# Performance work log

Hardware: AMD Instinct MI355X
Metric: run time of the kernel (lower is better)

## Reference

```python
import jax, jax.numpy as jnp
import numpy as np

SIZE = (64, 64, 64)
NSTEPS = 7
_EPS = 1e-4


def _skew(w):
    z = jnp.zeros_like(w[:, 0])
    return jnp.stack([
        jnp.stack([z, -w[:, 2], w[:, 1]], -1),
        jnp.stack([w[:, 2], z, -w[:, 0]], -1),
        jnp.stack([-w[:, 1], w[:, 0], z], -1)], -2)


def _abc(theta):
    t2 = theta * theta
    small = theta < _EPS
    ts = jnp.where(small, 1.0, theta)
    A = jnp.where(small, 1.0 - t2 / 6.0, jnp.sin(ts) / ts)
    B = jnp.where(small, 0.5 - t2 / 24.0, (1.0 - jnp.cos(ts)) / (ts * ts))
    C = jnp.where(small, 1.0 / 6.0 - t2 / 120.0, (ts - jnp.sin(ts)) / (ts ** 3))
    return A, B, C


def se3_exp(xi):
    # xi: (N,6) = [v | w]; Rodrigues closed form -> (N,4,4)
    v, w = xi[:, :3], xi[:, 3:]
    theta = jnp.linalg.norm(w, axis=-1)
    A, B, C = _abc(theta)
    Wm = _skew(w)
    W2 = Wm @ Wm
    I = jnp.eye(3, dtype=xi.dtype)
    R = I + A[:, None, None] * Wm + B[:, None, None] * W2
    V = I + B[:, None, None] * Wm + C[:, None, None] * W2
    t = jnp.einsum('nij,nj->ni', V, v)
    top = jnp.concatenate([R, t[:, :, None]], -1)
    bottom = jnp.broadcast_to(jnp.array([0., 0., 0., 1.], xi.dtype), (xi.shape[0], 1, 4))
    return jnp.concatenate([top, bottom], 1)


def se3_log(M):
    # M: (N,4,4) -> (N,6) = [v | w]
    R = M[:, :3, :3]
    t = M[:, :3, 3]
    tr = jnp.trace(R, axis1=1, axis2=2)
    cos = jnp.clip((tr - 1.0) * 0.5, -1.0 + 1e-6, 1.0 - 1e-6)
    theta = jnp.arccos(cos)
    small = theta < _EPS
    ts = jnp.where(small, 1.0, theta)
    t2 = theta * theta
    fac = jnp.where(small, 1.0 + t2 / 6.0, ts / jnp.sin(ts))
    S = 0.5 * (R - jnp.swapaxes(R, 1, 2))
    w = jnp.stack([S[:, 2, 1], S[:, 0, 2], S[:, 1, 0]], -1) * fac[:, None]
    Wm = _skew(w)
    W2 = Wm @ Wm
    A, B, _ = _abc(theta)
    coef = jnp.where(small, 1.0 / 12.0, (1.0 - A / (2.0 * B)) / jnp.where(small, 1.0, t2))
    I = jnp.eye(3, dtype=M.dtype)
    Vinv = I - 0.5 * Wm + coef[:, None, None] * W2
    v = jnp.einsum('nij,nj->ni', Vinv, t)
    return jnp.concatenate([v, w], -1)


def _grid_points():
    # replicates NSETransformer grid: (2*i - (s-1)) / (max(size)-1), flattened (N,3)
    m = float(max(SIZE) - 1)
    ax = [(2.0 * jnp.arange(s, dtype=jnp.float32) - (s - 1)) / m for s in SIZE]
    g = jnp.stack(jnp.meshgrid(*ax, indexing='ij'), -1)  # (D,H,W,3)
    return g.reshape(-1, 3)


def _trilinear(src, coords):
    # src: (C,D,H,W); coords: (N,3) as (x,y,z) in [-1,1]; align_corners=True, border padding
    C, D, H, W = src.shape
    gx = jnp.clip((coords[:, 0] + 1.0) * 0.5 * (W - 1), 0.0, W - 1.0)
    gy = jnp.clip((coords[:, 1] + 1.0) * 0.5 * (H - 1), 0.0, H - 1.0)
    gz = jnp.clip((coords[:, 2] + 1.0) * 0.5 * (D - 1), 0.0, D - 1.0)
    x0 = jnp.floor(gx); y0 = jnp.floor(gy); z0 = jnp.floor(gz)
    fx, fy, fz = gx - x0, gy - y0, gz - z0
    x0i = x0.astype(jnp.int32); x1i = jnp.minimum(x0i + 1, W - 1)
    y0i = y0.astype(jnp.int32); y1i = jnp.minimum(y0i + 1, H - 1)
    z0i = z0.astype(jnp.int32); z1i = jnp.minimum(z0i + 1, D - 1)

    def g(zi, yi, xi):
        return src[:, zi, yi, xi]  # (C,N)

    out = (g(z0i, y0i, x0i) * (1 - fz) * (1 - fy) * (1 - fx)
           + g(z0i, y0i, x1i) * (1 - fz) * (1 - fy) * fx
           + g(z0i, y1i, x0i) * (1 - fz) * fy * (1 - fx)
           + g(z0i, y1i, x1i) * (1 - fz) * fy * fx
           + g(z1i, y0i, x0i) * fz * (1 - fy) * (1 - fx)
           + g(z1i, y0i, x1i) * fz * (1 - fy) * fx
           + g(z1i, y1i, x0i) * fz * fy * (1 - fx)
           + g(z1i, y1i, x1i) * fz * fy * fx)
    return out.T  # (N,C)


def setup_inputs() -> dict:
    key = jax.random.key(0)
    vec = jax.random.normal(key, (1, 6) + SIZE, dtype=jnp.float32) * 0.4
    return {"vec": vec}


def reference(vec):
    D, H, W = SIZE
    scale = 1.0 / (2 ** NSTEPS)
    vec_f = jnp.transpose(vec, (0, 2, 3, 4, 1)).reshape(-1, 6) * scale  # (N,6)
    mulMat = se3_exp(vec_f)  # (N,4,4)
    pts = _grid_points()  # (N,3) in (d0,d1,d2) order
    m = float(max(SIZE) - 1)
    denom = jnp.array([(s - 1) / m for s in SIZE], jnp.float32)
    for _ in range(NSTEPS):
        # SE3.act(mulMat, grid points)
        new_loc = jnp.einsum('nij,nj->ni', mulMat[:, :3, :3], pts) + mulMat[:, :3, 3]
        samp = (new_loc / denom)[:, ::-1]  # reorder [2,1,0] -> (x,y,z)
        src = vec_f.reshape(D, H, W, 6).transpose(3, 0, 1, 2)  # (6,D,H,W)
        interp = _trilinear(src, samp)  # (N,6)
        Mat2 = se3_exp(interp)
        mulMat = Mat2 @ mulMat
        vec_f = se3_log(mulMat)
    return vec_f
```

## Files before the change

### kernel.cpp

```cpp
#include <hip/hip_runtime.h>
#include <math.h>

#define DSZ   64
#define NVOX  (DSZ*DSZ*DSZ)
#define NSTEP 7

__device__ __forceinline__ float rcp_f(float x)  { return __builtin_amdgcn_rcpf(x); }
__device__ __forceinline__ float rsq_f(float x)  { return __builtin_amdgcn_rsqf(x); }

__device__ __forceinline__ void se3_exp_dev(const float xi[6], float R[9], float t[3]) {
    float vx = xi[0], vy = xi[1], vz = xi[2];
    float wx = xi[3], wy = xi[4], wz = xi[5];
    float t2 = wx*wx + wy*wy + wz*wz;
    float t2c = fmaxf(t2, 1e-20f);
    float it    = rsq_f(t2c);
    float theta = t2c*it;
    float s = __sinf(theta), c = __cosf(theta);
    float it2 = it*it;
    float A = s*it;
    float B = (1.0f - c)*it2;
    float C = (theta - s)*it2*it;
    bool sm = t2 < 1e-6f;
    A = sm ? 1.0f - t2*(1.0f/6.0f)            : A;
    B = sm ? 0.5f - t2*(1.0f/24.0f)           : B;
    C = sm ? (1.0f/6.0f) - t2*(1.0f/120.0f)   : C;

    float xx = wx*wx, yy = wy*wy, zz = wz*wz;
    float xy = wx*wy, xz = wx*wz, yz = wy*wz;
    R[0] = 1.0f - B*(yy+zz);
    R[1] = -A*wz + B*xy;
    R[2] =  A*wy + B*xz;
    R[3] =  A*wz + B*xy;
    R[4] = 1.0f - B*(xx+zz);
    R[5] = -A*wx + B*yz;
    R[6] = -A*wy + B*xz;
    R[7] =  A*wx + B*yz;
    R[8] = 1.0f - B*(xx+yy);
    float V0 = 1.0f - C*(yy+zz);
    float V1 = -B*wz + C*xy;
    float V2 =  B*wy + C*xz;
    float V3 =  B*wz + C*xy;
    float V4 = 1.0f - C*(xx+zz);
    float V5 = -B*wx + C*yz;
    float V6 = -B*wy + C*xz;
    float V7 =  B*wx + C*yz;
    float V8 = 1.0f - C*(xx+yy);
    t[0] = V0*vx + V1*vy + V2*vz;
    t[1] = V3*vx + V4*vy + V5*vz;
    t[2] = V6*vx + V7*vy + V8*vz;
}

__device__ __forceinline__ void se3_log_dev(const float R[9], const float t[3], float out[6]) {
    float tr = R[0] + R[4] + R[8];
    float cs = (tr - 1.0f)*0.5f;
    cs = fminf(fmaxf(cs, -1.0f + 1e-6f), 1.0f - 1e-6f);
    float theta = acosf(cs);
    float t2 = theta*theta;
    float ss2 = 1.0f - cs*cs;
    float isn = rsq_f(ss2);
    float fac = theta*isn;
    float sn  = ss2*isn;
    float coef = (1.0f - 0.5f*sn*theta*rcp_f(1.0f - cs)) * rcp_f(t2);
    bool sm = theta < 1e-3f;
    fac  = sm ? 1.0f + t2*(1.0f/6.0f) : fac;
    coef = sm ? (1.0f/12.0f)          : coef;

    float wx = 0.5f*(R[7]-R[5])*fac;
    float wy = 0.5f*(R[2]-R[6])*fac;
    float wz = 0.5f*(R[3]-R[1])*fac;
    float xx = wx*wx, yy = wy*wy, zz = wz*wz;
    float xy = wx*wy, xz = wx*wz, yz = wy*wz;
    float V0 = 1.0f - coef*(yy+zz);
    float V1 =  0.5f*wz + coef*xy;
    float V2 = -0.5f*wy + coef*xz;
    float V3 = -0.5f*wz + coef*xy;
    float V4 = 1.0f - coef*(xx+zz);
    float V5 =  0.5f*wx + coef*yz;
    float V6 =  0.5f*wy + coef*xz;
    float V7 = -0.5f*wx + coef*yz;
    float V8 = 1.0f - coef*(xx+yy);
    out[0] = V0*t[0] + V1*t[1] + V2*t[2];
    out[1] = V3*t[0] + V4*t[1] + V5*t[2];
    out[2] = V6*t[0] + V7*t[1] + V8*t[2];
    out[3] = wx; out[4] = wy; out[5] = wz;
}

__global__ __launch_bounds__(256) void init_kernel(const float* __restrict__ in,
                                                   float* __restrict__ vec) {
    int n = blockIdx.x*256 + threadIdx.x;
    const float scale = 1.0f/128.0f;
    float xi[6];
#pragma unroll
    for (int c = 0; c < 6; ++c) xi[c] = in[c*NVOX + n]*scale;
    float2* vp = reinterpret_cast<float2*>(vec + (size_t)n*6);
    vp[0] = make_float2(xi[0], xi[1]);
    vp[1] = make_float2(xi[2], xi[3]);
    vp[2] = make_float2(xi[4], xi[5]);
}

__global__ __launch_bounds__(256) void step_kernel(const float* __restrict__ vin,
                                                   float* __restrict__ vout) {
    int n = blockIdx.x*256 + threadIdx.x;

    const float2* v2 = reinterpret_cast<const float2*>(vin);
    float2 o0 = v2[n*3], o1 = v2[n*3+1], o2 = v2[n*3+2];
    float xi_own[6] = {o0.x, o0.y, o1.x, o1.y, o2.x, o2.y};
    float Rm[9], tm[3];
    se3_exp_dev(xi_own, Rm, tm);

    int k = n & 63, j = (n >> 6) & 63, i = n >> 12;
    const float inv63 = 1.0f/63.0f;
    float p0 = (float)(2*i - 63)*inv63;
    float p1 = (float)(2*j - 63)*inv63;
    float p2 = (float)(2*k - 63)*inv63;

    float nl0 = Rm[0]*p0 + Rm[1]*p1 + Rm[2]*p2 + tm[0];
    float nl1 = Rm[3]*p0 + Rm[4]*p1 + Rm[5]*p2 + tm[1];
    float nl2 = Rm[6]*p0 + Rm[7]*p1 + Rm[8]*p2 + tm[2];

    float gx = fminf(fmaxf((nl2 + 1.0f)*0.5f*63.0f, 0.0f), 63.0f);
    float gy = fminf(fmaxf((nl1 + 1.0f)*0.5f*63.0f, 0.0f), 63.0f);
    float gz = fminf(fmaxf((nl0 + 1.0f)*0.5f*63.0f, 0.0f), 63.0f);
    float x0f = floorf(gx), y0f = floorf(gy), z0f = floorf(gz);
    float fx = gx - x0f, fy = gy - y0f, fz = gz - z0f;
    int x0 = (int)x0f, y0 = (int)y0f, z0 = (int)z0f;
    int x1 = min(x0 + 1, 63), y1 = min(y0 + 1, 63), z1 = min(z0 + 1, 63);

    float w000 = (1.0f-fz)*(1.0f-fy)*(1.0f-fx);
    float w001 = (1.0f-fz)*(1.0f-fy)*fx;
    float w010 = (1.0f-fz)*fy*(1.0f-fx);
    float w011 = (1.0f-fz)*fy*fx;
    float w100 = fz*(1.0f-fy)*(1.0f-fx);
    float w101 = fz*(1.0f-fy)*fx;
    float w110 = fz*fy*(1.0f-fx);
    float w111 = fz*fy*fx;

    float acc0 = 0.f, acc1 = 0.f, acc2 = 0.f, acc3 = 0.f, acc4 = 0.f, acc5 = 0.f;
#define CORNER(zz_, yy_, xx_, ww_)                                              \
    {                                                                           \
        int b = ((((zz_) << 6) | (yy_)) << 6 | (xx_))*3;                        \
        float2 a = v2[b], bb = v2[b+1], cc = v2[b+2];                           \
        acc0 += (ww_)*a.x;  acc1 += (ww_)*a.y;                                  \
        acc2 += (ww_)*bb.x; acc3 += (ww_)*bb.y;                                 \
        acc4 += (ww_)*cc.x; acc5 += (ww_)*cc.y;                                 \
    }
    CORNER(z0, y0, x0, w000)
    CORNER(z0, y0, x1, w001)
    CORNER(z0, y1, x0, w010)
    CORNER(z0, y1, x1, w011)
    CORNER(z1, y0, x0, w100)
    CORNER(z1, y0, x1, w101)
    CORNER(z1, y1, x0, w110)
    CORNER(z1, y1, x1, w111)
#undef CORNER

    float interp[6] = {acc0, acc1, acc2, acc3, acc4, acc5};
    float R2[9], t2v[3];
    se3_exp_dev(interp, R2, t2v);

    float Rn[9], tn[3];
    Rn[0] = R2[0]*Rm[0] + R2[1]*Rm[3] + R2[2]*Rm[6];
    Rn[1] = R2[0]*Rm[1] + R2[1]*Rm[4] + R2[2]*Rm[7];
    Rn[2] = R2[0]*Rm[2] + R2[1]*Rm[5] + R2[2]*Rm[8];
    Rn[3] = R2[3]*Rm[0] + R2[4]*Rm[3] + R2[5]*Rm[6];
    Rn[4] = R2[3]*Rm[1] + R2[4]*Rm[4] + R2[5]*Rm[7];
    Rn[5] = R2[3]*Rm[2] + R2[4]*Rm[5] + R2[5]*Rm[8];
    Rn[6] = R2[6]*Rm[0] + R2[7]*Rm[3] + R2[8]*Rm[6];
    Rn[7] = R2[6]*Rm[1] + R2[7]*Rm[4] + R2[8]*Rm[7];
    Rn[8] = R2[6]*Rm[2] + R2[7]*Rm[5] + R2[8]*Rm[8];
    tn[0] = R2[0]*tm[0] + R2[1]*tm[1] + R2[2]*tm[2] + t2v[0];
    tn[1] = R2[3]*tm[0] + R2[4]*tm[1] + R2[5]*tm[2] + t2v[1];
    tn[2] = R2[6]*tm[0] + R2[7]*tm[1] + R2[8]*tm[2] + t2v[2];

    float out6[6];
    se3_log_dev(Rn, tn, out6);
    float2* op = reinterpret_cast<float2*>(vout + (size_t)n*6);
    op[0] = make_float2(out6[0], out6[1]);
    op[1] = make_float2(out6[2], out6[3]);
    op[2] = make_float2(out6[4], out6[5]);
}

extern "C" void kernel_launch(void* const* d_in, const int* in_sizes, int n_in,
                              void* d_out, int out_size, void* d_ws, size_t ws_size,
                              hipStream_t stream) {
    (void)in_sizes; (void)n_in; (void)out_size; (void)ws_size;
    const float* in = (const float*)d_in[0];
    float* out  = (float*)d_out;
    float* vecA = (float*)d_ws;

    dim3 blk(256), grid(NVOX/256);
    init_kernel<<<grid, blk, 0, stream>>>(in, vecA);

    const float* cur = vecA;
    for (int s = 1; s <= NSTEP; ++s) {
        float* dst = (s & 1) ? out : vecA;
        step_kernel<<<grid, blk, 0, stream>>>(cur, dst);
        cur = dst;
    }
}
```

Baseline: 72.78 us.

## Fuse init into first step and pad intermediate state to 8 floats

Removes the separate init kernel: the first step now reads the planar input directly and applies the scale after interpolating, so one launch and one full-volume pass are saved. Intermediate buffers are padded to 8 floats per voxel so each corner gather uses two 16-byte float4 loads instead of three float2 loads. The padding raises workspace use and write bandwidth, and the first step's planar gathers touch six separate cache lines per corner.

Measured after the change: 82.07 us. +12.8%, slower.

```diff
diff --git a/kernel.cpp b/kernel.cpp
--- a/kernel.cpp
+++ b/kernel.cpp
@@ -4,6 +4,7 @@
 #define DSZ   64
 #define NVOX  (DSZ*DSZ*DSZ)
 #define NSTEP 7
+#define SCALE (1.0f/128.0f)
 
 __device__ __forceinline__ float rcp_f(float x)  { return __builtin_amdgcn_rcpf(x); }
 __device__ __forceinline__ float rsq_f(float x)  { return __builtin_amdgcn_rsqf(x); }
@@ -85,26 +86,22 @@
     out[3] = wx; out[4] = wy; out[5] = wz;
 }
 
-__global__ __launch_bounds__(256) void init_kernel(const float* __restrict__ in,
-                                                   float* __restrict__ vec) {
-    int n = blockIdx.x*256 + threadIdx.x;
-    const float scale = 1.0f/128.0f;
-    float xi[6];
-#pragma unroll
-    for (int c = 0; c < 6; ++c) xi[c] = in[c*NVOX + n]*scale;
-    float2* vp = reinterpret_cast<float2*>(vec + (size_t)n*6);
-    vp[0] = make_float2(xi[0], xi[1]);
-    vp[1] = make_float2(xi[2], xi[3]);
-    vp[2] = make_float2(xi[4], xi[5]);
-}
-
+template<int MODE>
 __global__ __launch_bounds__(256) void step_kernel(const float* __restrict__ vin,
                                                    float* __restrict__ vout) {
     int n = blockIdx.x*256 + threadIdx.x;
 
-    const float2* v2 = reinterpret_cast<const float2*>(vin);
-    float2 o0 = v2[n*3], o1 = v2[n*3+1], o2 = v2[n*3+2];
-    float xi_own[6] = {o0.x, o0.y, o1.x, o1.y, o2.x, o2.y};
+    float xi_own[6];
+    if constexpr (MODE == 0) {
+#pragma unroll
+        for (int c = 0; c < 6; ++c) xi_own[c] = vin[c*NVOX + n]*SCALE;
+    } else {
+        const float4* v4 = reinterpret_cast<const float4*>(vin);
+        float4 a = v4[n*2], b = v4[n*2+1];
+        xi_own[0]=a.x; xi_own[1]=a.y; xi_own[2]=a.z;
+        xi_own[3]=a.w; xi_own[4]=b.x; xi_own[5]=b.y;
+    }
+
     float Rm[9], tm[3];
     se3_exp_dev(xi_own, Rm, tm);
 
@@ -136,23 +133,45 @@
     float w111 = fz*fy*fx;
 
     float acc0 = 0.f, acc1 = 0.f, acc2 = 0.f, acc3 = 0.f, acc4 = 0.f, acc5 = 0.f;
+    if constexpr (MODE == 0) {
+#define CORNER0(zz_, yy_, xx_, ww_)                                             \
+        {                                                                       \
+            int b = (((zz_) << 6) | (yy_)) << 6 | (xx_);                        \
+            acc0 += (ww_)*vin[b];             acc1 += (ww_)*vin[NVOX + b];      \
+            acc2 += (ww_)*vin[2*NVOX + b];    acc3 += (ww_)*vin[3*NVOX + b];    \
+            acc4 += (ww_)*vin[4*NVOX + b];    acc5 += (ww_)*vin[5*NVOX + b];    \
+        }
+        CORNER0(z0, y0, x0, w000)
+        CORNER0(z0, y0, x1, w001)
+        CORNER0(z0, y1, x0, w010)
+        CORNER0(z0, y1, x1, w011)
+        CORNER0(z1, y0, x0, w100)
+        CORNER0(z1, y0, x1, w101)
+        CORNER0(z1, y1, x0, w110)
+        CORNER0(z1, y1, x1, w111)
+#undef CORNER0
+        acc0 *= SCALE; acc1 *= SCALE; acc2 *= SCALE;
+        acc3 *= SCALE; acc4 *= SCALE; acc5 *= SCALE;
+    } else {
+        const float4* v4 = reinterpret_cast<const float4*>(vin);
 #define CORNER(zz_, yy_, xx_, ww_)                                              \
-    {                                                                           \
-        int b = ((((zz_) << 6) | (yy_)) << 6 | (xx_))*3;                        \
-        float2 a = v2[b], bb = v2[b+1], cc = v2[b+2];                           \
-        acc0 += (ww_)*a.x;  acc1 += (ww_)*a.y;                                  \
-        acc2 += (ww_)*bb.x; acc3 += (ww_)*bb.y;                                 \
-        acc4 += (ww_)*cc.x; acc5 += (ww_)*cc.y;                                 \
+        {                                                                       \
+            int b = ((((zz_) << 6) | (yy_)) << 6 | (xx_))*2;                    \
+            float4 a = v4[b], bb = v4[b+1];                                     \
+            acc0 += (ww_)*a.x;  acc1 += (ww_)*a.y;                              \
+            acc2 += (ww_)*a.z;  acc3 += (ww_)*a.w;                              \
+            acc4 += (ww_)*bb.x; acc5 += (ww_)*bb.y;                             \
+        }
+        CORNER(z0, y0, x0, w000)
+        CORNER(z0, y0, x1, w001)
+        CORNER(z0, y1, x0, w010)
+        CORNER(z0, y1, x1, w011)
+        CORNER(z1, y0, x0, w100)
+        CORNER(z1, y0, x1, w101)
+        CORNER(z1, y1, x0, w110)
+        CORNER(z1, y1, x1, w111)
+#undef CORNER
     }
-    CORNER(z0, y0, x0, w000)
-    CORNER(z0, y0, x1, w001)
-    CORNER(z0, y1, x0, w010)
-    CORNER(z0, y1, x1, w011)
-    CORNER(z1, y0, x0, w100)
-    CORNER(z1, y0, x1, w101)
-    CORNER(z1, y1, x0, w110)
-    CORNER(z1, y1, x1, w111)
-#undef CORNER
 
     float interp[6] = {acc0, acc1, acc2, acc3, acc4, acc5};
     float R2[9], t2v[3];
@@ -174,10 +193,17 @@
 
     float out6[6];
     se3_log_dev(Rn, tn, out6);
-    float2* op = reinterpret_cast<float2*>(vout + (size_t)n*6);
-    op[0] = make_float2(out6[0], out6[1]);
-    op[1] = make_float2(out6[2], out6[3]);
-    op[2] = make_float2(out6[4], out6[5]);
+
+    if constexpr (MODE == 2) {
+        float2* op = reinterpret_cast<float2*>(vout + (size_t)n*6);
+        op[0] = make_float2(out6[0], out6[1]);
+        op[1] = make_float2(out6[2], out6[3]);
+        op[2] = make_float2(out6[4], out6[5]);
+    } else {
+        float4* op = reinterpret_cast<float4*>(vout) + (size_t)n*2;
+        op[0] = make_float4(out6[0], out6[1], out6[2], out6[3]);
+        op[1] = make_float4(out6[4], out6[5], 0.0f, 0.0f);
+    }
 }
 
 extern "C" void kernel_launch(void* const* d_in, const int* in_sizes, int n_in,
@@ -185,16 +211,17 @@
                               hipStream_t stream) {
     (void)in_sizes; (void)n_in; (void)out_size; (void)ws_size;
     const float* in = (const float*)d_in[0];
-    float* out  = (float*)d_out;
-    float* vecA = (float*)d_ws;
+    float* out = (float*)d_out;
+    char*  ws  = (char*)d_ws;
+    float* bufP0 = (float*)ws;
+    float* bufP1 = (float*)(ws + (size_t)NVOX*8*sizeof(float));
 
     dim3 blk(256), grid(NVOX/256);
-    init_kernel<<<grid, blk, 0, stream>>>(in, vecA);
-
-    const float* cur = vecA;
-    for (int s = 1; s <= NSTEP; ++s) {
-        float* dst = (s & 1) ? out : vecA;
-        step_kernel<<<grid, blk, 0, stream>>>(cur, dst);
-        cur = dst;
-    }
-}
+    step_kernel<0><<<grid, blk, 0, stream>>>(in, bufP0);
+    step_kernel<1><<<grid, blk, 0, stream>>>(bufP0, bufP1);
+    step_kernel<1><<<grid, blk, 0, stream>>>(bufP1, bufP0);
+    step_kernel<1><<<grid, blk, 0, stream>>>(bufP0, bufP1);
+    step_kernel<1><<<grid, blk, 0, stream>>>(bufP1, bufP0);
+    step_kernel<1><<<grid, blk, 0, stream>>>(bufP0, bufP1);
+    step_kernel<2><<<grid, blk, 0, stream>>>(bufP1, out);
+}
```
